# Optimization experiments

Measured on AMD Instinct MI355X. Metric: run time of the kernel, lower is better.

The kernel has to match this reference:

```python
import jax, jax.numpy as jnp
import numpy as np

N_NODES = 200000
D_IN = 256
D_OUT = 256
B = 4096
K1 = 25   # layer-1 fanout
K2 = 10   # layer-2 fanout
M = B * (1 + K2)  # layer-1 node set size: batch centers + their sampled neighbors


def setup_inputs() -> dict:
    key = jax.random.key(0)
    k1, k2, k3, k4, k5, k6 = jax.random.split(key, 6)
    features = jax.random.normal(k1, (N_NODES, D_IN), dtype=jnp.float32)
    # SageLayer weights: [out, 2*in] (concat path, gcn=False); small kaiming-like scale
    W1 = jax.random.normal(k2, (D_OUT, 2 * D_IN), dtype=jnp.float32) * 0.05
    W2 = jax.random.normal(k3, (D_OUT, 2 * D_OUT), dtype=jnp.float32) * 0.05
    nodes_batch = jax.random.randint(k4, (B,), 0, N_NODES, dtype=jnp.int64)
    neigh2 = jax.random.randint(k5, (B, K2), 0, N_NODES, dtype=jnp.int64)
    neigh1 = jax.random.randint(k6, (M, K1), 0, N_NODES, dtype=jnp.int64)
    return {"features": features, "W1": W1, "W2": W2,
            "nodes_batch": nodes_batch, "neigh2": neigh2, "neigh1": neigh1}


def reference(features, W1, W2, nodes_batch, neigh2, neigh1):
    # Layer-1 node set: centers first, then their sampled layer-2 neighbors.
    l1_nodes = jnp.concatenate([nodes_batch, neigh2.reshape(-1)])  # [M]
    # ---- layer 1: MEAN aggregate over K1 sampled neighbors (gather + mean) ----
    agg1 = jnp.mean(features[neigh1], axis=1)          # [M, K1, D_IN] -> [M, D_IN]
    self1 = features[l1_nodes]                         # [M, D_IN]
    # SageLayer: relu(W.mm(cat(self, agg).T)).T == relu(cat @ W.T)
    h1 = jax.nn.relu(jnp.concatenate([self1, agg1], axis=1) @ W1.T)  # [M, D_OUT]
    # ---- layer 2: centers are h1[:B]; neighbor embeddings are h1[B:] in blocks of K2 ----
    nb = nodes_batch.shape[0]
    agg2 = jnp.mean(h1[nb:].reshape(nb, -1, h1.shape[1]), axis=1)    # [B, D_OUT]
    h2 = jax.nn.relu(jnp.concatenate([h1[:nb], agg2], axis=1) @ W2.T)  # [B, D_OUT]
    return h2
```

## Files before the change

### kernel.cpp

```cpp
#include <hip/hip_runtime.h>
#include <hip/hip_bf16.h>

typedef __attribute__((ext_vector_type(8))) short bf16x8;
typedef __attribute__((ext_vector_type(4))) float f32x4;
typedef __attribute__((ext_vector_type(2))) float f32x2;

#define B_SZ   4096
#define K1     25
#define K2     10
#define M_L1   45056
#define D      256
#define K_DIM  512
#define N_NODES 200000

#define AS1 __attribute__((address_space(1)))
#define AS3 __attribute__((address_space(3)))

static __device__ __forceinline__ unsigned short f2bf(float f) {
    union { float f; unsigned u; } v; v.f = f;
    return (unsigned short)((v.u + 0x7fffu + ((v.u >> 16) & 1u)) >> 16);
}
static __device__ __forceinline__ float bf2f(unsigned short h) {
    union { unsigned u; float f; } v; v.u = ((unsigned)h) << 16;
    return v.f;
}

__global__ __launch_bounds__(256)
void convert_all(const float* __restrict__ f, unsigned* __restrict__ f8,
                 const float* __restrict__ W1, const float* __restrict__ W2,
                 unsigned short* __restrict__ W1b, unsigned short* __restrict__ W2b) {
    const size_t i = ((size_t)blockIdx.x * 256 + threadIdx.x) * 8;
    const float4 a = *(const float4*)(f + i);
    const float4 b = *(const float4*)(f + i + 4);
    unsigned u0 = 0, u1 = 0;
    u0 = __builtin_amdgcn_cvt_pk_fp8_f32(a.x, a.y, u0, false);
    u0 = __builtin_amdgcn_cvt_pk_fp8_f32(a.z, a.w, u0, true);
    u1 = __builtin_amdgcn_cvt_pk_fp8_f32(b.x, b.y, u1, false);
    u1 = __builtin_amdgcn_cvt_pk_fp8_f32(b.z, b.w, u1, true);
    uint2 r; r.x = u0; r.y = u1;
    *(uint2*)(f8 + (i >> 2)) = r;
    const int j = blockIdx.x * 256 + threadIdx.x;
    if (j < D * K_DIM) {
        W1b[j] = f2bf(W1[j]);
        W2b[j] = f2bf(W2[j]);
    }
}

__global__ __launch_bounds__(256)
void agg1_kernel(const float* __restrict__ feat,
                 const unsigned* __restrict__ f8,
                 const int* __restrict__ nodes_batch,
                 const int* __restrict__ neigh2,
                 const int* __restrict__ neigh1,
                 unsigned short* __restrict__ X1) {
    const int wave = threadIdx.x >> 6;
    const int lane = threadIdx.x & 63;
    const int m = (blockIdx.x << 2) + wave;
    const int self_node = (m < B_SZ) ? nodes_batch[m] : neigh2[m - B_SZ];
    const int* nb = neigh1 + (size_t)m * K1;

    int idxv = (lane < K1) ? nb[lane] : 0;
    const float4 s = *(const float4*)(feat + (size_t)self_node * D + (lane << 2));

    unsigned q[K1];
    #pragma unroll
    for (int j = 0; j < K1; ++j) {
        const int node = __shfl(idxv, j);
        q[j] = f8[(size_t)node * (D / 4) + lane];
    }

    float a0 = 0.f, a1 = 0.f, a2 = 0.f, a3 = 0.f;
    #pragma unroll
    for (int j = 0; j < K1; ++j) {
        const f32x2 lo = __builtin_amdgcn_cvt_pk_f32_fp8(q[j], false);
        const f32x2 hi = __builtin_amdgcn_cvt_pk_f32_fp8(q[j], true);
        a0 += lo.x; a1 += lo.y; a2 += hi.x; a3 += hi.y;
    }
    const float inv = 1.0f / (float)K1;

    unsigned short* xr = X1 + (size_t)m * K_DIM;
    *(ushort4*)(xr + (lane << 2)) =
        make_ushort4(f2bf(s.x), f2bf(s.y), f2bf(s.z), f2bf(s.w));
    *(ushort4*)(xr + D + (lane << 2)) =
        make_ushort4(f2bf(a0 * inv), f2bf(a1 * inv), f2bf(a2 * inv), f2bf(a3 * inv));
}

__global__ __launch_bounds__(256)
void agg2_kernel(const unsigned short* __restrict__ h1,
                 unsigned short* __restrict__ X2) {
    const int wave = threadIdx.x >> 6;
    const int lane = threadIdx.x & 63;
    const int b = (blockIdx.x << 2) + wave;
    const ushort4 s = *(const ushort4*)(h1 + (size_t)b * D + (lane << 2));
    float sx = 0.f, sy = 0.f, sz = 0.f, sw = 0.f;
    #pragma unroll
    for (int k = 0; k < K2; ++k) {
        const ushort4 v = *(const ushort4*)(h1 + (size_t)(B_SZ + b * K2 + k) * D + (lane << 2));
        sx += bf2f(v.x); sy += bf2f(v.y); sz += bf2f(v.z); sw += bf2f(v.w);
    }
    const float inv = 1.0f / (float)K2;
    unsigned short* xr = X2 + (size_t)b * K_DIM;
    *(ushort4*)(xr + (lane << 2)) = s;
    *(ushort4*)(xr + D + (lane << 2)) =
        make_ushort4(f2bf(sx * inv), f2bf(sy * inv), f2bf(sz * inv), f2bf(sw * inv));
}

template<int BM, bool OUT_BF16>
__global__ __launch_bounds__(256)
void gemm_relu(const unsigned short* __restrict__ A,
               const unsigned short* __restrict__ W,
               void* __restrict__ Cout) {
    constexpr int MFR = BM / 16;
    constexpr int ACALLS = BM / 8;
    __shared__ unsigned short As[2][BM * 64];
    __shared__ unsigned short Bs[2][256 * 64];
    const int tid  = threadIdx.x;
    const int w    = tid >> 6, lane = tid & 63;
    const int quad = lane >> 4, l16 = lane & 15;
    const int wn   = w << 6;
    const size_t row0 = (size_t)blockIdx.x * BM;

    const int srow   = lane >> 3;
    const int schunk = ((lane & 7) ^ srow) << 3;
    const unsigned short* aG = A + (row0 + srow) * K_DIM + schunk;
    const unsigned short* bG = W + (size_t)srow * K_DIM + schunk;

    f32x4 acc[MFR][4];
    #pragma unroll
    for (int i = 0; i < MFR; ++i)
        #pragma unroll
        for (int j = 0; j < 4; ++j)
            acc[i][j] = (f32x4){0.f, 0.f, 0.f, 0.f};

    auto stage = [&](int buf, int k0) {
        #pragma unroll
        for (int c = w; c < ACALLS; c += 4)
            __builtin_amdgcn_global_load_lds(
                (const AS1 void*)(aG + (size_t)(c * 8) * K_DIM + k0),
                (AS3 void*)(&As[buf][c * 512]), 16, 0, 0);
        #pragma unroll
        for (int c = w; c < 32; c += 4)
            __builtin_amdgcn_global_load_lds(
                (const AS1 void*)(bG + (size_t)(c * 8) * K_DIM + k0),
                (AS3 void*)(&Bs[buf][c * 512]), 16, 0, 0);
    };

    auto compute = [&](int buf) {
        #pragma unroll
        for (int ks = 0; ks < 2; ++ks) {
            bf16x8 af[MFR], bfr[4];
            #pragma unroll
            for (int i = 0; i < MFR; ++i) {
                const int row = i * 16 + l16;
                af[i] = *(const bf16x8*)&As[buf][row * 64 + ((((ks << 2) + quad) ^ (l16 & 7)) << 3)];
            }
            #pragma unroll
            for (int i = 0; i < 4; ++i) {
                const int row = wn + i * 16 + l16;
                bfr[i] = *(const bf16x8*)&Bs[buf][row * 64 + ((((ks << 2) + quad) ^ (l16 & 7)) << 3)];
            }
            #pragma unroll
            for (int mi = 0; mi < MFR; ++mi)
                #pragma unroll
                for (int ni = 0; ni < 4; ++ni)
                    acc[mi][ni] = __builtin_amdgcn_mfma_f32_16x16x32_bf16(
                        af[mi], bfr[ni], acc[mi][ni], 0, 0, 0);
        }
    };

    stage(0, 0);
    asm volatile("s_waitcnt vmcnt(0)" ::: "memory");
    __syncthreads();
    #pragma unroll
    for (int t = 0; t < 7; ++t) {
        stage((t & 1) ^ 1, (t + 1) << 6);
        compute(t & 1);
        asm volatile("s_waitcnt vmcnt(0)" ::: "memory");
        __syncthreads();
    }
    compute(1);

    #pragma unroll
    for (int mi = 0; mi < MFR; ++mi) {
        #pragma unroll
        for (int ni = 0; ni < 4; ++ni) {
            #pragma unroll
            for (int r = 0; r < 4; ++r) {
                const size_t gm = row0 + mi * 16 + quad * 4 + r;
                const size_t gn = (size_t)wn + ni * 16 + l16;
                float v = acc[mi][ni][r];
                v = v > 0.f ? v : 0.f;
                if (OUT_BF16)
                    ((unsigned short*)Cout)[gm * D + gn] = f2bf(v);
                else
                    ((float*)Cout)[gm * D + gn] = v;
            }
        }
    }
}

extern "C" void kernel_launch(void* const* d_in, const int* in_sizes, int n_in,
                              void* d_out, int out_size, void* d_ws, size_t ws_size,
                              hipStream_t stream) {
    const float* feat        = (const float*)d_in[0];
    const float* W1          = (const float*)d_in[1];
    const float* W2          = (const float*)d_in[2];
    const int*   nodes_batch = (const int*)d_in[3];
    const int*   neigh2      = (const int*)d_in[4];
    const int*   neigh1      = (const int*)d_in[5];
    float* out = (float*)d_out;

    char* ws = (char*)d_ws;
    unsigned*       f8   = (unsigned*)(ws);
    unsigned short* X1   = (unsigned short*)(ws + 51200000);
    unsigned short* h1   = (unsigned short*)(ws + 51200000 + 46137344);
    unsigned short* X2   = (unsigned short*)(ws + 51200000 + 46137344 + 23068672);
    unsigned short* W1b  = (unsigned short*)(ws + 51200000 + 46137344 + 23068672 + 4194304);
    unsigned short* W2b  = (unsigned short*)(ws + 51200000 + 46137344 + 23068672 + 4194304 + 262144);

    convert_all<<<25000, 256, 0, stream>>>(feat, f8, W1, W2, W1b, W2b);
    agg1_kernel<<<M_L1 / 4, 256, 0, stream>>>(feat, f8, nodes_batch, neigh2, neigh1, X1);
    gemm_relu<64, true><<<M_L1 / 64, 256, 0, stream>>>(X1, W1b, h1);
    agg2_kernel<<<B_SZ / 4, 256, 0, stream>>>(h1, X2);
    gemm_relu<16, false><<<B_SZ / 16, 256, 0, stream>>>(X2, W2b, out);
}
```

Measured before the change: 383.5 us.

## Fuse neighbor aggregation into GEMM prologues, keeping A tiles in LDS

Merges the layer-1 gather/mean with its GEMM and the layer-2 mean with its GEMM. Each block builds its swizzled concatenated [self|agg] tile directly in LDS, so the X1 and X2 intermediates are never written to or read back from global memory, and two launches disappear. Layer 1 now uses 512-thread blocks with a 64x512 bf16 A tile held entirely in LDS, which raises LDS use per block and may reduce occupancy. The gather latency is no longer overlapped with other blocks' GEMM work within a block, and there are only 704 blocks in layer 1.

```diff
diff --git a/kernel.cpp b/kernel.cpp
--- a/kernel.cpp
+++ b/kernel.cpp
@@ -46,157 +46,207 @@
     }
 }
 
-__global__ __launch_bounds__(256)
-void agg1_kernel(const float* __restrict__ feat,
-                 const unsigned* __restrict__ f8,
-                 const int* __restrict__ nodes_batch,
-                 const int* __restrict__ neigh2,
-                 const int* __restrict__ neigh1,
-                 unsigned short* __restrict__ X1) {
-    const int wave = threadIdx.x >> 6;
-    const int lane = threadIdx.x & 63;
-    const int m = (blockIdx.x << 2) + wave;
-    const int self_node = (m < B_SZ) ? nodes_batch[m] : neigh2[m - B_SZ];
-    const int* nb = neigh1 + (size_t)m * K1;
-
-    int idxv = (lane < K1) ? nb[lane] : 0;
-    const float4 s = *(const float4*)(feat + (size_t)self_node * D + (lane << 2));
-
-    unsigned q[K1];
-    #pragma unroll
-    for (int j = 0; j < K1; ++j) {
-        const int node = __shfl(idxv, j);
-        q[j] = f8[(size_t)node * (D / 4) + lane];
-    }
-
-    float a0 = 0.f, a1 = 0.f, a2 = 0.f, a3 = 0.f;
-    #pragma unroll
-    for (int j = 0; j < K1; ++j) {
-        const f32x2 lo = __builtin_amdgcn_cvt_pk_f32_fp8(q[j], false);
-        const f32x2 hi = __builtin_amdgcn_cvt_pk_f32_fp8(q[j], true);
-        a0 += lo.x; a1 += lo.y; a2 += hi.x; a3 += hi.y;
-    }
-    const float inv = 1.0f / (float)K1;
-
-    unsigned short* xr = X1 + (size_t)m * K_DIM;
-    *(ushort4*)(xr + (lane << 2)) =
-        make_ushort4(f2bf(s.x), f2bf(s.y), f2bf(s.z), f2bf(s.w));
-    *(ushort4*)(xr + D + (lane << 2)) =
-        make_ushort4(f2bf(a0 * inv), f2bf(a1 * inv), f2bf(a2 * inv), f2bf(a3 * inv));
-}
-
-__global__ __launch_bounds__(256)
-void agg2_kernel(const unsigned short* __restrict__ h1,
-                 unsigned short* __restrict__ X2) {
-    const int wave = threadIdx.x >> 6;
-    const int lane = threadIdx.x & 63;
-    const int b = (blockIdx.x << 2) + wave;
-    const ushort4 s = *(const ushort4*)(h1 + (size_t)b * D + (lane << 2));
-    float sx = 0.f, sy = 0.f, sz = 0.f, sw = 0.f;
-    #pragma unroll
-    for (int k = 0; k < K2; ++k) {
-        const ushort4 v = *(const ushort4*)(h1 + (size_t)(B_SZ + b * K2 + k) * D + (lane << 2));
-        sx += bf2f(v.x); sy += bf2f(v.y); sz += bf2f(v.z); sw += bf2f(v.w);
-    }
-    const float inv = 1.0f / (float)K2;
-    unsigned short* xr = X2 + (size_t)b * K_DIM;
-    *(ushort4*)(xr + (lane << 2)) = s;
-    *(ushort4*)(xr + D + (lane << 2)) =
-        make_ushort4(f2bf(sx * inv), f2bf(sy * inv), f2bf(sz * inv), f2bf(sw * inv));
-}
-
-template<int BM, bool OUT_BF16>
-__global__ __launch_bounds__(256)
-void gemm_relu(const unsigned short* __restrict__ A,
-               const unsigned short* __restrict__ W,
-               void* __restrict__ Cout) {
-    constexpr int MFR = BM / 16;
-    constexpr int ACALLS = BM / 8;
-    __shared__ unsigned short As[2][BM * 64];
+__global__ __launch_bounds__(512)
+void fused_l1(const float* __restrict__ feat,
+              const unsigned* __restrict__ f8,
+              const int* __restrict__ nodes_batch,
+              const int* __restrict__ neigh2,
+              const int* __restrict__ neigh1,
+              const unsigned short* __restrict__ W,
+              unsigned short* __restrict__ h1) {
+    __shared__ unsigned short As[64 * 512];
     __shared__ unsigned short Bs[2][256 * 64];
     const int tid  = threadIdx.x;
     const int w    = tid >> 6, lane = tid & 63;
     const int quad = lane >> 4, l16 = lane & 15;
-    const int wn   = w << 6;
-    const size_t row0 = (size_t)blockIdx.x * BM;
+    const size_t row0 = (size_t)blockIdx.x * 64;
 
     const int srow   = lane >> 3;
     const int schunk = ((lane & 7) ^ srow) << 3;
-    const unsigned short* aG = A + (row0 + srow) * K_DIM + schunk;
     const unsigned short* bG = W + (size_t)srow * K_DIM + schunk;
 
-    f32x4 acc[MFR][4];
-    #pragma unroll
-    for (int i = 0; i < MFR; ++i)
+    #pragma unroll
+    for (int c = w; c < 32; c += 8)
+        __builtin_amdgcn_global_load_lds(
+            (const AS1 void*)(bG + (size_t)(c * 8) * K_DIM),
+            (AS3 void*)(&Bs[0][c * 512]), 16, 0, 0);
+
+    #pragma unroll 2
+    for (int rr = 0; rr < 8; ++rr) {
+        const int r = (w << 3) + rr;
+        const int m = (int)row0 + r;
+        const int self_node = (m < B_SZ) ? nodes_batch[m] : neigh2[m - B_SZ];
+        const int* nb = neigh1 + (size_t)m * K1;
+        int idxv = (lane < K1) ? nb[lane] : 0;
+        const float4 s = *(const float4*)(feat + (size_t)self_node * D + (lane << 2));
+        unsigned q[K1];
+        #pragma unroll
+        for (int j = 0; j < K1; ++j) {
+            const int node = __shfl(idxv, j);
+            q[j] = f8[(size_t)node * (D / 4) + lane];
+        }
+        float a0 = 0.f, a1 = 0.f, a2 = 0.f, a3 = 0.f;
+        #pragma unroll
+        for (int j = 0; j < K1; ++j) {
+            const f32x2 lo = __builtin_amdgcn_cvt_pk_f32_fp8(q[j], false);
+            const f32x2 hi = __builtin_amdgcn_cvt_pk_f32_fp8(q[j], true);
+            a0 += lo.x; a1 += lo.y; a2 += hi.x; a3 += hi.y;
+        }
+        const float inv = 1.0f / (float)K1;
+        const int e0 = lane << 2;
+        const int p0 = (e0 >> 3) ^ (r & 7);
+        *(ushort4*)&As[r * 512 + (p0 << 3) + (e0 & 7)] =
+            make_ushort4(f2bf(s.x), f2bf(s.y), f2bf(s.z), f2bf(s.w));
+        const int e1 = D + (lane << 2);
+        const int p1 = (e1 >> 3) ^ (r & 7);
+        *(ushort4*)&As[r * 512 + (p1 << 3) + (e1 & 7)] =
+            make_ushort4(f2bf(a0 * inv), f2bf(a1 * inv), f2bf(a2 * inv), f2bf(a3 * inv));
+    }
+
+    asm volatile("s_waitcnt vmcnt(0)" ::: "memory");
+    __syncthreads();
+
+    const int wm = (w >> 2) << 5;
+    const int wn = (w & 3) << 6;
+    f32x4 acc[2][4];
+    #pragma unroll
+    for (int i = 0; i < 2; ++i)
         #pragma unroll
         for (int j = 0; j < 4; ++j)
             acc[i][j] = (f32x4){0.f, 0.f, 0.f, 0.f};
 
-    auto stage = [&](int buf, int k0) {
-        #pragma unroll
-        for (int c = w; c < ACALLS; c += 4)
-            __builtin_amdgcn_global_load_lds(
-                (const AS1 void*)(aG + (size_t)(c * 8) * K_DIM + k0),
-                (AS3 void*)(&As[buf][c * 512]), 16, 0, 0);
-        #pragma unroll
-        for (int c = w; c < 32; c += 4)
-            __builtin_amdgcn_global_load_lds(
-                (const AS1 void*)(bG + (size_t)(c * 8) * K_DIM + k0),
-                (AS3 void*)(&Bs[buf][c * 512]), 16, 0, 0);
-    };
-
-    auto compute = [&](int buf) {
+    for (int t = 0; t < 8; ++t) {
+        if (t < 7) {
+            #pragma unroll
+            for (int c = w; c < 32; c += 8)
+                __builtin_amdgcn_global_load_lds(
+                    (const AS1 void*)(bG + (size_t)(c * 8) * K_DIM + ((t + 1) << 6)),
+                    (AS3 void*)(&Bs[(t + 1) & 1][c * 512]), 16, 0, 0);
+        }
         #pragma unroll
         for (int ks = 0; ks < 2; ++ks) {
-            bf16x8 af[MFR], bfr[4];
-            #pragma unroll
-            for (int i = 0; i < MFR; ++i) {
-                const int row = i * 16 + l16;
-                af[i] = *(const bf16x8*)&As[buf][row * 64 + ((((ks << 2) + quad) ^ (l16 & 7)) << 3)];
+            bf16x8 af[2], bfr[4];
+            #pragma unroll
+            for (int i = 0; i < 2; ++i) {
+                const int row = wm + i * 16 + l16;
+                const int ch  = (t << 3) + (ks << 2) + quad;
+                af[i] = *(const bf16x8*)&As[row * 512 + ((ch ^ (row & 7)) << 3)];
             }
             #pragma unroll
             for (int i = 0; i < 4; ++i) {
                 const int row = wn + i * 16 + l16;
-                bfr[i] = *(const bf16x8*)&Bs[buf][row * 64 + ((((ks << 2) + quad) ^ (l16 & 7)) << 3)];
-            }
-            #pragma unroll
-            for (int mi = 0; mi < MFR; ++mi)
+                bfr[i] = *(const bf16x8*)&Bs[t & 1][row * 64 + ((((ks << 2) + quad) ^ (l16 & 7)) << 3)];
+            }
+            #pragma unroll
+            for (int mi = 0; mi < 2; ++mi)
                 #pragma unroll
                 for (int ni = 0; ni < 4; ++ni)
                     acc[mi][ni] = __builtin_amdgcn_mfma_f32_16x16x32_bf16(
                         af[mi], bfr[ni], acc[mi][ni], 0, 0, 0);
         }
-    };
-
-    stage(0, 0);
+        asm volatile("s_waitcnt vmcnt(0)" ::: "memory");
+        __syncthreads();
+    }
+
+    #pragma unroll
+    for (int mi = 0; mi < 2; ++mi)
+        #pragma unroll
+        for (int ni = 0; ni < 4; ++ni)
+            #pragma unroll
+            for (int rg = 0; rg < 4; ++rg) {
+                const size_t gm = row0 + wm + mi * 16 + quad * 4 + rg;
+                const size_t gn = (size_t)wn + ni * 16 + l16;
+                float v = acc[mi][ni][rg];
+                v = v > 0.f ? v : 0.f;
+                h1[gm * D + gn] = f2bf(v);
+            }
+}
+
+__global__ __launch_bounds__(256)
+void fused_l2(const unsigned short* __restrict__ h1,
+              const unsigned short* __restrict__ W,
+              float* __restrict__ out) {
+    __shared__ unsigned short As[16 * 512];
+    __shared__ unsigned short Bs[2][256 * 64];
+    const int tid  = threadIdx.x;
+    const int w    = tid >> 6, lane = tid & 63;
+    const int quad = lane >> 4, l16 = lane & 15;
+    const size_t row0 = (size_t)blockIdx.x * 16;
+
+    const int srow   = lane >> 3;
+    const int schunk = ((lane & 7) ^ srow) << 3;
+    const unsigned short* bG = W + (size_t)srow * K_DIM + schunk;
+
+    #pragma unroll
+    for (int c = w; c < 32; c += 4)
+        __builtin_amdgcn_global_load_lds(
+            (const AS1 void*)(bG + (size_t)(c * 8) * K_DIM),
+            (AS3 void*)(&Bs[0][c * 512]), 16, 0, 0);
+
+    #pragma unroll
+    for (int rr = 0; rr < 4; ++rr) {
+        const int r = (w << 2) + rr;
+        const size_t b = row0 + r;
+        const ushort4 sv = *(const ushort4*)&h1[b * D + (lane << 2)];
+        float a0 = 0.f, a1 = 0.f, a2 = 0.f, a3 = 0.f;
+        #pragma unroll
+        for (int k = 0; k < K2; ++k) {
+            const ushort4 v = *(const ushort4*)&h1[(size_t)(B_SZ + b * K2 + k) * D + (lane << 2)];
+            a0 += bf2f(v.x); a1 += bf2f(v.y); a2 += bf2f(v.z); a3 += bf2f(v.w);
+        }
+        const float inv = 1.0f / (float)K2;
+        const int e0 = lane << 2;
+        const int p0 = (e0 >> 3) ^ (r & 7);
+        *(ushort4*)&As[r * 512 + (p0 << 3) + (e0 & 7)] = sv;
+        const int e1 = D + (lane << 2);
+        const int p1 = (e1 >> 3) ^ (r & 7);
+        *(ushort4*)&As[r * 512 + (p1 << 3) + (e1 & 7)] =
+            make_ushort4(f2bf(a0 * inv), f2bf(a1 * inv), f2bf(a2 * inv), f2bf(a3 * inv));
+    }
+
     asm volatile("s_waitcnt vmcnt(0)" ::: "memory");
     __syncthreads();
-    #pragma unroll
-    for (int t = 0; t < 7; ++t) {
-        stage((t & 1) ^ 1, (t + 1) << 6);
-        compute(t & 1);
+
+    const int wn = w << 6;
+    f32x4 acc[4];
+    #pragma unroll
+    for (int j = 0; j < 4; ++j) acc[j] = (f32x4){0.f, 0.f, 0.f, 0.f};
+
+    for (int t = 0; t < 8; ++t) {
+        if (t < 7) {
+            #pragma unroll
+            for (int c = w; c < 32; c += 4)
+                __builtin_amdgcn_global_load_lds(
+                    (const AS1 void*)(bG + (size_t)(c * 8) * K_DIM + ((t + 1) << 6)),
+                    (AS3 void*)(&Bs[(t + 1) & 1][c * 512]), 16, 0, 0);
+        }
+        #pragma unroll
+        for (int ks = 0; ks < 2; ++ks) {
+            const int ch = (t << 3) + (ks << 2) + quad;
+            const bf16x8 af = *(const bf16x8*)&As[l16 * 512 + ((ch ^ (l16 & 7)) << 3)];
+            bf16x8 bfr[4];
+            #pragma unroll
+            for (int i = 0; i < 4; ++i) {
+                const int row = wn + i * 16 + l16;
+                bfr[i] = *(const bf16x8*)&Bs[t & 1][row * 64 + ((((ks << 2) + quad) ^ (l16 & 7)) << 3)];
+            }
+            #pragma unroll
+            for (int ni = 0; ni < 4; ++ni)
+                acc[ni] = __builtin_amdgcn_mfma_f32_16x16x32_bf16(af, bfr[ni], acc[ni], 0, 0, 0);
+        }
         asm volatile("s_waitcnt vmcnt(0)" ::: "memory");
         __syncthreads();
     }
-    compute(1);
-
-    #pragma unroll
-    for (int mi = 0; mi < MFR; ++mi) {
-        #pragma unroll
-        for (int ni = 0; ni < 4; ++ni) {
-            #pragma unroll
-            for (int r = 0; r < 4; ++r) {
-                const size_t gm = row0 + mi * 16 + quad * 4 + r;
-                const size_t gn = (size_t)wn + ni * 16 + l16;
-                float v = acc[mi][ni][r];
-                v = v > 0.f ? v : 0.f;
-                if (OUT_BF16)
-                    ((unsigned short*)Cout)[gm * D + gn] = f2bf(v);
-                else
-                    ((float*)Cout)[gm * D + gn] = v;
-            }
-        }
-    }
+
+    #pragma unroll
+    for (int ni = 0; ni < 4; ++ni)
+        #pragma unroll
+        for (int rg = 0; rg < 4; ++rg) {
+            const size_t gm = row0 + quad * 4 + rg;
+            const size_t gn = (size_t)wn + ni * 16 + l16;
+            float v = acc[ni][rg];
+            out[gm * D + gn] = v > 0.f ? v : 0.f;
+        }
 }
 
 extern "C" void kernel_launch(void* const* d_in, const int* in_sizes, int n_in,
@@ -211,16 +261,12 @@
     float* out = (float*)d_out;
 
     char* ws = (char*)d_ws;
-    unsigned*       f8   = (unsigned*)(ws);
-    unsigned short* X1   = (unsigned short*)(ws + 51200000);
-    unsigned short* h1   = (unsigned short*)(ws + 51200000 + 46137344);
-    unsigned short* X2   = (unsigned short*)(ws + 51200000 + 46137344 + 23068672);
-    unsigned short* W1b  = (unsigned short*)(ws + 51200000 + 46137344 + 23068672 + 4194304);
-    unsigned short* W2b  = (unsigned short*)(ws + 51200000 + 46137344 + 23068672 + 4194304 + 262144);
+    unsigned*       f8  = (unsigned*)(ws);
+    unsigned short* h1  = (unsigned short*)(ws + 51200000);
+    unsigned short* W1b = (unsigned short*)(ws + 51200000 + 23068672);
+    unsigned short* W2b = (unsigned short*)(ws + 51200000 + 23068672 + 262144);
 
     convert_all<<<25000, 256, 0, stream>>>(feat, f8, W1, W2, W1b, W2b);
-    agg1_kernel<<<M_L1 / 4, 256, 0, stream>>>(feat, f8, nodes_batch, neigh2, neigh1, X1);
-    gemm_relu<64, true><<<M_L1 / 64, 256, 0, stream>>>(X1, W1b, h1);
-    agg2_kernel<<<B_SZ / 4, 256, 0, stream>>>(h1, X2);
-    gemm_relu<16, false><<<B_SZ / 16, 256, 0, stream>>>(X2, W2b, out);
-}
+    fused_l1<<<M_L1 / 64, 512, 0, stream>>>(feat, f8, nodes_batch, neigh2, neigh1, W1b, h1);
+    fused_l2<<<B_SZ / 16, 256, 0, stream>>>(h1, W2b, out);
+}
```

Measured after the change: 365.4 us. -4.7%, faster.
